# Kernel optimization log

Hardware: AMD Instinct MI355X
Metric: run time of the kernel (lower is better)

## Reference

```python
import jax, jax.numpy as jnp
import numpy as np

V, H, B, T = 8192, 1024, 64, 128

def setup_inputs() -> dict:
    key = jax.random.key(0)
    ks = jax.random.split(key, 7)
    s = 1.0 / np.sqrt(H)                     # torch LSTMCell/Linear default init bound
    xg = np.sqrt(6.0 / (H + V))              # xavier_uniform for fc_out.weight
    return {
        "h0":   jax.random.normal(ks[0], (B, H), jnp.float32),
        "W_ih": jax.random.uniform(ks[1], (4 * H, V), jnp.float32, -s, s),
        "W_hh": jax.random.uniform(ks[2], (4 * H, H), jnp.float32, -s, s),
        "b_ih": jax.random.uniform(ks[3], (4 * H,), jnp.float32, -s, s),
        "b_hh": jax.random.uniform(ks[4], (4 * H,), jnp.float32, -s, s),
        "W_fc": jax.random.uniform(ks[5], (V, H), jnp.float32, -xg, xg),
        "b_fc": jax.random.uniform(ks[6], (V,), jnp.float32, -s, s),
        "max_length": T,
    }

def reference(h0, W_ih, W_hh, b_ih, b_hh, W_fc, b_fc, max_length):
    B_, H_ = h0.shape
    V_ = W_ih.shape[1]
    # hidden state fed to the cell is ALWAYS features[1] (h0) in the original code,
    # so its contribution to the gates is constant across timesteps.
    hh = h0 @ W_hh.T + b_hh + b_ih  # (B, 4H)

    def step(carry, _):
        x, c = carry                          # x: (B,V) accumulated one-hots, c: (B,H)
        gates = x @ W_ih.T + hh               # (B, 4H), torch gate order i,f,g,o
        i, f, g, o = jnp.split(gates, 4, axis=1)
        c = jax.nn.sigmoid(f) * c + jax.nn.sigmoid(i) * jnp.tanh(g)
        h = jax.nn.sigmoid(o) * jnp.tanh(c)
        out = h @ W_fc.T + b_fc               # (B, V)
        idx = jnp.argmax(out, axis=1)
        x = x + jax.nn.one_hot(idx, V_, dtype=x.dtype)  # +1 at argmax (cumulative)
        return (x, c), out

    init = (jnp.zeros((B_, V_), h0.dtype), jnp.zeros((B_, H_), h0.dtype))
    _, outs = jax.lax.scan(step, init, None, length=max_length)  # (T, B, V)
    return jnp.transpose(outs, (1, 2, 0))  # (B, V, T)
```

## Files before the change

kernel.cpp:

```cpp
#include <hip/hip_runtime.h>
#include <math.h>

#define VDIM 8192
#define HDIM 1024
#define BDIM 64
#define TDIM 128
#define H4   4096
#define TCH  16

__device__ __forceinline__ float sigf(float x){ return 1.0f/(1.0f + expf(-x)); }

__device__ __forceinline__ unsigned long long packmax(float v, int vidx){
    unsigned int u = __float_as_uint(v);
    u = (u & 0x80000000u) ? ~u : (u | 0x80000000u);
    return ((unsigned long long)u << 32) | (unsigned int)(VDIM - 1 - vidx);
}

__global__ void __launch_bounds__(256)
hh_kernel(const float* __restrict__ h0, const float* __restrict__ W_hh,
          const float* __restrict__ b_ih, const float* __restrict__ b_hh,
          float* __restrict__ gates)
{
    int blk = blockIdx.x;
    int b = blk >> 4;
    int j = (blk & 15)*256 + threadIdx.x;
    const float* hr = h0 + (size_t)b*HDIM;
    const float* wr = W_hh + (size_t)j*HDIM;
    float s = 0.f;
    for (int k = 0; k < HDIM; k += 4){
        float4 hv = *(const float4*)(hr + k);
        float4 wv = *(const float4*)(wr + k);
        s = fmaf(hv.x, wv.x, s); s = fmaf(hv.y, wv.y, s);
        s = fmaf(hv.z, wv.z, s); s = fmaf(hv.w, wv.w, s);
    }
    gates[(size_t)b*H4 + j] = s + b_ih[j] + b_hh[j];
}

__global__ void __launch_bounds__(256)
cell0_kernel(const float* __restrict__ gates, float* __restrict__ cbuf,
             float* __restrict__ hbuf)
{
    int b = blockIdx.x, u = threadIdx.x*4;
    const float* gb = gates + (size_t)b*H4;
    float4 gi = *(const float4*)(gb + u);
    float4 gf = *(const float4*)(gb + 1024 + u);
    float4 gg = *(const float4*)(gb + 2048 + u);
    float4 go = *(const float4*)(gb + 3072 + u);
    (void)gf;
    float4 c4, h4;
    c4.x = sigf(gi.x)*tanhf(gg.x); c4.y = sigf(gi.y)*tanhf(gg.y);
    c4.z = sigf(gi.z)*tanhf(gg.z); c4.w = sigf(gi.w)*tanhf(gg.w);
    h4.x = sigf(go.x)*tanhf(c4.x); h4.y = sigf(go.y)*tanhf(c4.y);
    h4.z = sigf(go.z)*tanhf(c4.z); h4.w = sigf(go.w)*tanhf(c4.w);
    *(float4*)(cbuf + (size_t)b*HDIM + u) = c4;
    *(float4*)(hbuf + (size_t)b*HDIM + u) = h4;
}

__global__ void __launch_bounds__(256)
tr_kernel(const float* __restrict__ W, float* __restrict__ WT)
{
    __shared__ float tile[64][65];
    const int jb = blockIdx.x * 64;
    const int vb = blockIdx.y * 64;
    const int tx = threadIdx.x & 63;
    const int ty = threadIdx.x >> 6;
    #pragma unroll
    for (int k = 0; k < 64; k += 4)
        tile[ty + k][tx] = W[(size_t)(jb + ty + k)*VDIM + vb + tx];
    __syncthreads();
    #pragma unroll
    for (int k = 0; k < 64; k += 4)
        WT[(size_t)(vb + ty + k)*H4 + jb + tx] = tile[tx][ty + k];
}

__global__ void __launch_bounds__(512, 2)
fc_kernel(const float* __restrict__ W_fc, const float* __restrict__ b_fc,
          const float* __restrict__ hbuf, float* __restrict__ out,
          float* __restrict__ stage,
          unsigned long long* __restrict__ pmax, int t)
{
    __shared__ float buf[8*2048];
    __shared__ unsigned long long bmax[512];
    const int tid = threadIdx.x;
    const int blk = blockIdx.x;
    const int vbase = blk * 32;
    const int g  = tid >> 5;
    const int s  = tid & 31;
    const int b0 = (s >> 2) * 8;
    const int v0 = (s & 3) * 8;
    const int k0 = g * 64;

    float acc[8][8];
    #pragma unroll
    for (int i=0;i<8;++i){
        #pragma unroll
        for (int j=0;j<8;++j) acc[i][j] = 0.f;
    }

    const float* hb = hbuf + (size_t)b0*HDIM + k0;
    const float* wb = W_fc + (size_t)(vbase + v0)*HDIM + k0;

    #pragma unroll 2
    for (int kc = 0; kc < 16; ++kc){
        float4 h4[8], w4[8];
        #pragma unroll
        for (int i=0;i<8;++i) h4[i] = *(const float4*)(hb + (size_t)i*HDIM + kc*4);
        #pragma unroll
        for (int j=0;j<8;++j) w4[j] = *(const float4*)(wb + (size_t)j*HDIM + kc*4);
        #pragma unroll
        for (int i=0;i<8;++i){
            #pragma unroll
            for (int j=0;j<8;++j){
                acc[i][j] = fmaf(h4[i].x, w4[j].x, acc[i][j]);
                acc[i][j] = fmaf(h4[i].y, w4[j].y, acc[i][j]);
                acc[i][j] = fmaf(h4[i].z, w4[j].z, acc[i][j]);
                acc[i][j] = fmaf(h4[i].w, w4[j].w, acc[i][j]);
            }
        }
    }

    for (int half = 8; half >= 1; half >>= 1){
        if (g >= half && g < 2*half){
            float* bp = buf + (g - half)*2048;
            #pragma unroll
            for (int i=0;i<8;++i)
                #pragma unroll
                for (int j=0;j<8;++j) bp[(b0+i)*32 + v0 + j] = acc[i][j];
        }
        __syncthreads();
        if (g < half){
            const float* bp = buf + g*2048;
            #pragma unroll
            for (int i=0;i<8;++i)
                #pragma unroll
                for (int j=0;j<8;++j) acc[i][j] += bp[(b0+i)*32 + v0 + j];
        }
        __syncthreads();
    }
    if (g == 0){
        #pragma unroll
        for (int i=0;i<8;++i)
            #pragma unroll
            for (int j=0;j<8;++j) buf[(b0+i)*32 + v0 + j] = acc[i][j];
    }
    __syncthreads();

    {
        int b  = tid >> 3;
        int vv = (tid & 7) * 4;
        float4 r = *(float4*)(buf + b*32 + vv);
        int v = vbase + vv;
        r.x += b_fc[v]; r.y += b_fc[v+1]; r.z += b_fc[v+2]; r.w += b_fc[v+3];
        if (stage){
            *(float4*)(stage + (((size_t)(t & (TCH-1))*BDIM + b)*VDIM + v)) = r;
        } else {
            float* ob = out + ((size_t)b*VDIM + v)*TDIM + t;
            ob[0] = r.x; ob[TDIM] = r.y; ob[2*TDIM] = r.z; ob[3*TDIM] = r.w;
        }
        unsigned long long m  = packmax(r.x, v);
        unsigned long long m2 = packmax(r.y, v+1); if (m2 > m) m = m2;
        m2 = packmax(r.z, v+2); if (m2 > m) m = m2;
        m2 = packmax(r.w, v+3); if (m2 > m) m = m2;
        bmax[tid] = m;
        __syncthreads();
        if (tid < 64){
            unsigned long long mm = bmax[tid*8];
            #pragma unroll
            for (int q=1;q<8;++q){ unsigned long long z = bmax[tid*8+q]; if (z > mm) mm = z; }
            pmax[(size_t)tid*256 + blk] = mm;
        }
    }
}

__global__ void __launch_bounds__(256)
flush_kernel(const float* __restrict__ stage, float* __restrict__ out, int t0)
{
    const size_t n = (size_t)blockIdx.x*256 + threadIdx.x;
    const int b = (int)(n >> 13);
    const int v = (int)(n & (VDIM-1));
    const size_t st = (size_t)BDIM*VDIM;
    const float* sp = stage + (size_t)b*VDIM + v;
    float* op = out + ((size_t)b*VDIM + v)*TDIM + t0;
    float4 o0, o1, o2, o3;
    o0.x = sp[0*st];  o0.y = sp[1*st];  o0.z = sp[2*st];  o0.w = sp[3*st];
    o1.x = sp[4*st];  o1.y = sp[5*st];  o1.z = sp[6*st];  o1.w = sp[7*st];
    o2.x = sp[8*st];  o2.y = sp[9*st];  o2.z = sp[10*st]; o2.w = sp[11*st];
    o3.x = sp[12*st]; o3.y = sp[13*st]; o3.z = sp[14*st]; o3.w = sp[15*st];
    *(float4*)(op + 0)  = o0;
    *(float4*)(op + 4)  = o1;
    *(float4*)(op + 8)  = o2;
    *(float4*)(op + 12) = o3;
}

__global__ void __launch_bounds__(256)
cell_kernel(const float* __restrict__ W_ih, const float* __restrict__ W_ihT,
            float* __restrict__ gates, float* __restrict__ cbuf,
            float* __restrict__ hbuf, const unsigned long long* __restrict__ pmax)
{
    __shared__ float gbuf[H4];
    __shared__ unsigned long long red[256];
    const int b = blockIdx.x, tid = threadIdx.x;

    red[tid] = pmax[(size_t)b*256 + tid];
    __syncthreads();
    for (int st = 128; st; st >>= 1){
        if (tid < st){ if (red[tid+st] > red[tid]) red[tid] = red[tid+st]; }
        __syncthreads();
    }
    const int idx = VDIM - 1 - (int)(unsigned int)(red[0] & 0xffffffffULL);

    float* gb = gates + (size_t)b*H4;
    if (W_ihT){
        const float* row = W_ihT + (size_t)idx*H4;
        #pragma unroll
        for (int q = 0; q < 4; ++q){
            int j4 = q*1024 + tid*4;
            float4 wv = *(const float4*)(row + j4);
            float4 gv = *(const float4*)(gb + j4);
            gv.x += wv.x; gv.y += wv.y; gv.z += wv.z; gv.w += wv.w;
            *(float4*)(gb + j4) = gv;
            *(float4*)(gbuf + j4) = gv;
        }
    } else {
        #pragma unroll
        for (int q = 0; q < 16; ++q){
            int j = q*256 + tid;
            float gv = gb[j] + W_ih[(size_t)j*VDIM + idx];
            gb[j] = gv;
            gbuf[j] = gv;
        }
    }
    __syncthreads();

    int u = tid*4;
    float4 gi = *(float4*)(gbuf + u);
    float4 gf = *(float4*)(gbuf + 1024 + u);
    float4 gg = *(float4*)(gbuf + 2048 + u);
    float4 go = *(float4*)(gbuf + 3072 + u);
    float4 c4 = *(float4*)(cbuf + (size_t)b*HDIM + u);
    c4.x = sigf(gf.x)*c4.x + sigf(gi.x)*tanhf(gg.x);
    c4.y = sigf(gf.y)*c4.y + sigf(gi.y)*tanhf(gg.y);
    c4.z = sigf(gf.z)*c4.z + sigf(gi.z)*tanhf(gg.z);
    c4.w = sigf(gf.w)*c4.w + sigf(gi.w)*tanhf(gg.w);
    float4 h4;
    h4.x = sigf(go.x)*tanhf(c4.x); h4.y = sigf(go.y)*tanhf(c4.y);
    h4.z = sigf(go.z)*tanhf(c4.z); h4.w = sigf(go.w)*tanhf(c4.w);
    *(float4*)(cbuf + (size_t)b*HDIM + u) = c4;
    *(float4*)(hbuf + (size_t)b*HDIM + u) = h4;
}

extern "C" void kernel_launch(void* const* d_in, const int* in_sizes, int n_in,
                              void* d_out, int out_size, void* d_ws, size_t ws_size,
                              hipStream_t stream)
{
    const float* h0   = (const float*)d_in[0];
    const float* W_ih = (const float*)d_in[1];
    const float* W_hh = (const float*)d_in[2];
    const float* b_ih = (const float*)d_in[3];
    const float* b_hh = (const float*)d_in[4];
    const float* W_fc = (const float*)d_in[5];
    const float* b_fc = (const float*)d_in[6];
    float* out = (float*)d_out;

    float* gates = (float*)d_ws;
    float* cbuf  = gates + (size_t)BDIM*H4;
    float* hbuf  = cbuf  + (size_t)BDIM*HDIM;
    unsigned long long* pmax = (unsigned long long*)(hbuf + (size_t)BDIM*HDIM);

    size_t off = (size_t)BDIM*H4*4 + 2*(size_t)BDIM*HDIM*4 + (size_t)BDIM*256*8;
    const size_t STAGE_B = (size_t)TCH*BDIM*VDIM*4;
    const size_t WT_B    = (size_t)VDIM*H4*4;
    float* stage = nullptr;
    float* wT    = nullptr;
    if (ws_size >= off + STAGE_B){ stage = (float*)((char*)d_ws + off); off += STAGE_B; }
    if (ws_size >= off + WT_B)   { wT    = (float*)((char*)d_ws + off); off += WT_B; }

    hipLaunchKernelGGL(hh_kernel, dim3(1024), dim3(256), 0, stream,
                       h0, W_hh, b_ih, b_hh, gates);
    hipLaunchKernelGGL(cell0_kernel, dim3(64), dim3(256), 0, stream,
                       gates, cbuf, hbuf);
    if (wT){
        hipLaunchKernelGGL(tr_kernel, dim3(64, 128), dim3(256), 0, stream,
                           W_ih, wT);
    }

    for (int t = 0; t < TDIM; ++t){
        hipLaunchKernelGGL(fc_kernel, dim3(256), dim3(512), 0, stream,
                           W_fc, b_fc, hbuf, out, stage, pmax, t);
        if (stage && (t & (TCH-1)) == (TCH-1)){
            hipLaunchKernelGGL(flush_kernel, dim3(BDIM*VDIM/256), dim3(256), 0, stream,
                               stage, out, t - (TCH-1));
        }
        if (t < TDIM - 1){
            hipLaunchKernelGGL(cell_kernel, dim3(64), dim3(256), 0, stream,
                               W_ih, wT, gates, cbuf, hbuf, pmax);
        }
    }
}
```

Measured before the change: 7.292 ms.

## Fuse per-timestep kernels into one persistent cooperative kernel with grid syncs

Replaces the host loop of fc, flush and cell kernel launches per timestep with a single cooperative loop_kernel that runs all 128 timesteps. Grid-wide barriers separate the FC and argmax phase, the cell update and the periodic stage flush. This removes roughly 270 kernel launches and their inter-kernel gaps. In exchange it pays for two grid.sync calls per step, keeps all 256 blocks resident, and shares one block shape across phases that previously used different launch configurations. It falls back to the old path if the cooperative launch fails.

```diff
diff --git a/kernel.cpp b/kernel.cpp
--- a/kernel.cpp
+++ b/kernel.cpp
@@ -1,5 +1,8 @@
 #include <hip/hip_runtime.h>
+#include <hip/hip_cooperative_groups.h>
 #include <math.h>
+
+namespace cg = cooperative_groups;
 
 #define VDIM 8192
 #define HDIM 1024
@@ -73,11 +76,177 @@
         WT[(size_t)(vb + ty + k)*H4 + jb + tx] = tile[tx][ty + k];
 }
 
+__global__ void __launch_bounds__(512)
+loop_kernel(const float* __restrict__ W_fc, const float* __restrict__ b_fc,
+            const float* __restrict__ W_ihT, float* __restrict__ out,
+            float* __restrict__ stage, float* __restrict__ gates,
+            float* __restrict__ cbuf, float* __restrict__ hbuf,
+            unsigned long long* __restrict__ pmax)
+{
+    cg::grid_group grid = cg::this_grid();
+    __shared__ float buf[8*2048];
+    __shared__ unsigned long long bmax[512];
+
+    const int tid = threadIdx.x;
+    const int blk = blockIdx.x;
+    const int vbase = blk * 32;
+    const int g  = tid >> 5;
+    const int s  = tid & 31;
+    const int b0 = (s >> 2) * 8;
+    const int v0 = (s & 3) * 8;
+    const int k0 = g * 64;
+    const int cb = blk & 63;
+    const int cq = blk >> 6;
+
+    const float* hb = hbuf + (size_t)b0*HDIM + k0;
+    const float* wb = W_fc + (size_t)(vbase + v0)*HDIM + k0;
+
+    for (int t = 0; t < TDIM; ++t){
+        float acc[8][8];
+        #pragma unroll
+        for (int i=0;i<8;++i){
+            #pragma unroll
+            for (int j=0;j<8;++j) acc[i][j] = 0.f;
+        }
+
+        #pragma unroll 2
+        for (int kc = 0; kc < 16; ++kc){
+            float4 h4[8], w4[8];
+            #pragma unroll
+            for (int i=0;i<8;++i) h4[i] = *(const float4*)(hb + (size_t)i*HDIM + kc*4);
+            #pragma unroll
+            for (int j=0;j<8;++j) w4[j] = *(const float4*)(wb + (size_t)j*HDIM + kc*4);
+            #pragma unroll
+            for (int i=0;i<8;++i){
+                #pragma unroll
+                for (int j=0;j<8;++j){
+                    acc[i][j] = fmaf(h4[i].x, w4[j].x, acc[i][j]);
+                    acc[i][j] = fmaf(h4[i].y, w4[j].y, acc[i][j]);
+                    acc[i][j] = fmaf(h4[i].z, w4[j].z, acc[i][j]);
+                    acc[i][j] = fmaf(h4[i].w, w4[j].w, acc[i][j]);
+                }
+            }
+        }
+
+        for (int half = 8; half >= 1; half >>= 1){
+            if (g >= half && g < 2*half){
+                float* bp = buf + (g - half)*2048;
+                #pragma unroll
+                for (int i=0;i<8;++i)
+                    #pragma unroll
+                    for (int j=0;j<8;++j) bp[(b0+i)*32 + v0 + j] = acc[i][j];
+            }
+            __syncthreads();
+            if (g < half){
+                const float* bp = buf + g*2048;
+                #pragma unroll
+                for (int i=0;i<8;++i)
+                    #pragma unroll
+                    for (int j=0;j<8;++j) acc[i][j] += bp[(b0+i)*32 + v0 + j];
+            }
+            __syncthreads();
+        }
+        if (g == 0){
+            #pragma unroll
+            for (int i=0;i<8;++i)
+                #pragma unroll
+                for (int j=0;j<8;++j) buf[(b0+i)*32 + v0 + j] = acc[i][j];
+        }
+        __syncthreads();
+
+        {
+            int eb = tid >> 3;
+            int vv = (tid & 7) * 4;
+            float4 r = *(float4*)(buf + eb*32 + vv);
+            int v = vbase + vv;
+            r.x += b_fc[v]; r.y += b_fc[v+1]; r.z += b_fc[v+2]; r.w += b_fc[v+3];
+            *(float4*)(stage + (((size_t)(t & (TCH-1))*BDIM + eb)*VDIM + v)) = r;
+            unsigned long long m  = packmax(r.x, v);
+            unsigned long long m2 = packmax(r.y, v+1); if (m2 > m) m = m2;
+            m2 = packmax(r.z, v+2); if (m2 > m) m = m2;
+            m2 = packmax(r.w, v+3); if (m2 > m) m = m2;
+            bmax[tid] = m;
+            __syncthreads();
+            if (tid < 64){
+                unsigned long long mm = bmax[tid*8];
+                #pragma unroll
+                for (int q=1;q<8;++q){ unsigned long long z = bmax[tid*8+q]; if (z > mm) mm = z; }
+                pmax[(size_t)tid*256 + blk] = mm;
+            }
+        }
+
+        grid.sync();
+
+        if (t < TDIM - 1){
+            if (tid < 256) bmax[tid] = pmax[(size_t)cb*256 + tid];
+            __syncthreads();
+            for (int st = 128; st; st >>= 1){
+                if (tid < st){ if (bmax[tid+st] > bmax[tid]) bmax[tid] = bmax[tid+st]; }
+                __syncthreads();
+            }
+            const int idx = VDIM - 1 - (int)(unsigned int)(bmax[0] & 0xffffffffULL);
+
+            if (tid < 64){
+                const int u = cq*256 + tid*4;
+                const float* row = W_ihT + (size_t)idx*H4;
+                float* gb = gates + (size_t)cb*H4;
+                float4 gi = *(float4*)(gb + u);
+                float4 gf = *(float4*)(gb + 1024 + u);
+                float4 gg = *(float4*)(gb + 2048 + u);
+                float4 go = *(float4*)(gb + 3072 + u);
+                float4 wi = *(const float4*)(row + u);
+                float4 wf = *(const float4*)(row + 1024 + u);
+                float4 wg = *(const float4*)(row + 2048 + u);
+                float4 wo = *(const float4*)(row + 3072 + u);
+                gi.x += wi.x; gi.y += wi.y; gi.z += wi.z; gi.w += wi.w;
+                gf.x += wf.x; gf.y += wf.y; gf.z += wf.z; gf.w += wf.w;
+                gg.x += wg.x; gg.y += wg.y; gg.z += wg.z; gg.w += wg.w;
+                go.x += wo.x; go.y += wo.y; go.z += wo.z; go.w += wo.w;
+                *(float4*)(gb + u)        = gi;
+                *(float4*)(gb + 1024 + u) = gf;
+                *(float4*)(gb + 2048 + u) = gg;
+                *(float4*)(gb + 3072 + u) = go;
+                float4 c4 = *(float4*)(cbuf + (size_t)cb*HDIM + u);
+                c4.x = sigf(gf.x)*c4.x + sigf(gi.x)*tanhf(gg.x);
+                c4.y = sigf(gf.y)*c4.y + sigf(gi.y)*tanhf(gg.y);
+                c4.z = sigf(gf.z)*c4.z + sigf(gi.z)*tanhf(gg.z);
+                c4.w = sigf(gf.w)*c4.w + sigf(gi.w)*tanhf(gg.w);
+                float4 h4;
+                h4.x = sigf(go.x)*tanhf(c4.x); h4.y = sigf(go.y)*tanhf(c4.y);
+                h4.z = sigf(go.z)*tanhf(c4.z); h4.w = sigf(go.w)*tanhf(c4.w);
+                *(float4*)(cbuf + (size_t)cb*HDIM + u) = c4;
+                *(float4*)(hbuf + (size_t)cb*HDIM + u) = h4;
+            }
+        }
+
+        if ((t & (TCH-1)) == (TCH-1)){
+            const int t0 = t - (TCH-1);
+            for (int n = blk*512 + tid; n < BDIM*VDIM; n += 256*512){
+                const int fb = n >> 13;
+                const int fv = n & (VDIM-1);
+                const size_t st = (size_t)BDIM*VDIM;
+                const float* sp = stage + (size_t)fb*VDIM + fv;
+                float* op = out + ((size_t)fb*VDIM + fv)*TDIM + t0;
+                float4 o0, o1, o2, o3;
+                o0.x = sp[0*st];  o0.y = sp[1*st];  o0.z = sp[2*st];  o0.w = sp[3*st];
+                o1.x = sp[4*st];  o1.y = sp[5*st];  o1.z = sp[6*st];  o1.w = sp[7*st];
+                o2.x = sp[8*st];  o2.y = sp[9*st];  o2.z = sp[10*st]; o2.w = sp[11*st];
+                o3.x = sp[12*st]; o3.y = sp[13*st]; o3.z = sp[14*st]; o3.w = sp[15*st];
+                *(float4*)(op + 0)  = o0;
+                *(float4*)(op + 4)  = o1;
+                *(float4*)(op + 8)  = o2;
+                *(float4*)(op + 12) = o3;
+            }
+        }
+
+        grid.sync();
+    }
+}
+
 __global__ void __launch_bounds__(512, 2)
 fc_kernel(const float* __restrict__ W_fc, const float* __restrict__ b_fc,
           const float* __restrict__ hbuf, float* __restrict__ out,
-          float* __restrict__ stage,
-          unsigned long long* __restrict__ pmax, int t)
+          float* __restrict__ stage, unsigned long long* __restrict__ pmax, int t)
 {
     __shared__ float buf[8*2048];
     __shared__ unsigned long long bmax[512];
@@ -96,10 +265,8 @@
         #pragma unroll
         for (int j=0;j<8;++j) acc[i][j] = 0.f;
     }
-
     const float* hb = hbuf + (size_t)b0*HDIM + k0;
     const float* wb = W_fc + (size_t)(vbase + v0)*HDIM + k0;
-
     #pragma unroll 2
     for (int kc = 0; kc < 16; ++kc){
         float4 h4[8], w4[8];
@@ -118,7 +285,6 @@
             }
         }
     }
-
     for (int half = 8; half >= 1; half >>= 1){
         if (g >= half && g < 2*half){
             float* bp = buf + (g - half)*2048;
@@ -144,7 +310,6 @@
             for (int j=0;j<8;++j) buf[(b0+i)*32 + v0 + j] = acc[i][j];
     }
     __syncthreads();
-
     {
         int b  = tid >> 3;
         int vv = (tid & 7) * 4;
@@ -284,16 +449,29 @@
                            W_ih, wT);
     }
 
-    for (int t = 0; t < TDIM; ++t){
-        hipLaunchKernelGGL(fc_kernel, dim3(256), dim3(512), 0, stream,
-                           W_fc, b_fc, hbuf, out, stage, pmax, t);
-        if (stage && (t & (TCH-1)) == (TCH-1)){
-            hipLaunchKernelGGL(flush_kernel, dim3(BDIM*VDIM/256), dim3(256), 0, stream,
-                               stage, out, t - (TCH-1));
-        }
-        if (t < TDIM - 1){
-            hipLaunchKernelGGL(cell_kernel, dim3(64), dim3(256), 0, stream,
-                               W_ih, wT, gates, cbuf, hbuf, pmax);
-        }
-    }
-}
+    bool coop_done = false;
+    if (stage && wT){
+        void* args[] = { (void*)&W_fc, (void*)&b_fc, (void*)&wT, (void*)&out,
+                         (void*)&stage, (void*)&gates, (void*)&cbuf, (void*)&hbuf,
+                         (void*)&pmax };
+        hipError_t e = hipLaunchCooperativeKernel((const void*)loop_kernel,
+                                                  dim3(256), dim3(512),
+                                                  args, 0, stream);
+        if (e == hipSuccess) coop_done = true;
+    }
+
+    if (!coop_done){
+        for (int t = 0; t < TDIM; ++t){
+            hipLaunchKernelGGL(fc_kernel, dim3(256), dim3(512), 0, stream,
+                               W_fc, b_fc, hbuf, out, stage, pmax, t);
+            if (stage && (t & (TCH-1)) == (TCH-1)){
+                hipLaunchKernelGGL(flush_kernel, dim3(BDIM*VDIM/256), dim3(256), 0, stream,
+                                   stage, out, t - (TCH-1));
+            }
+            if (t < TDIM - 1){
+                hipLaunchKernelGGL(cell_kernel, dim3(64), dim3(256), 0, stream,
+                                   W_ih, wT, gates, cbuf, hbuf, pmax);
+            }
+        }
+    }
+}
```

New measurement: 14.33 ms. 1.96x slower.

## Split FC GEMV across 512 blocks and replace tree reduction with one-shot smem reduce

Applied to the files above, without the earlier changes.

The per-step FC kernel now has each block cover 16 vocabulary rows instead of 32, which doubles the grid to 512 blocks and halves per-thread accumulators to raise occupancy. The log-step shared-memory split-K reduction with many barriers is replaced by a single padded shared-memory dump followed by 256 threads each summing all 16 partials. The argmax partial buffer grows to 512 entries per batch row, and the cell kernel folds two entries per thread. In exchange, each h tile is re-read by twice as many blocks and the reduction uses more shared memory per block.

```diff
diff --git a/kernel.cpp b/kernel.cpp
--- a/kernel.cpp
+++ b/kernel.cpp
@@ -7,6 +7,8 @@
 #define TDIM 128
 #define H4   4096
 #define TCH  16
+#define NFC  512
+#define GS   1088
 
 __device__ __forceinline__ float sigf(float x){ return 1.0f/(1.0f + expf(-x)); }
 
@@ -73,28 +75,28 @@
         WT[(size_t)(vb + ty + k)*H4 + jb + tx] = tile[tx][ty + k];
 }
 
-__global__ void __launch_bounds__(512, 2)
+__global__ void __launch_bounds__(512, 4)
 fc_kernel(const float* __restrict__ W_fc, const float* __restrict__ b_fc,
           const float* __restrict__ hbuf, float* __restrict__ out,
           float* __restrict__ stage,
           unsigned long long* __restrict__ pmax, int t)
 {
-    __shared__ float buf[8*2048];
-    __shared__ unsigned long long bmax[512];
+    __shared__ float buf[16*GS];
+    __shared__ unsigned long long bmax[256];
     const int tid = threadIdx.x;
     const int blk = blockIdx.x;
-    const int vbase = blk * 32;
+    const int vbase = blk * 16;
     const int g  = tid >> 5;
     const int s  = tid & 31;
     const int b0 = (s >> 2) * 8;
-    const int v0 = (s & 3) * 8;
+    const int v0 = (s & 3) * 4;
     const int k0 = g * 64;
 
-    float acc[8][8];
+    float acc[8][4];
     #pragma unroll
     for (int i=0;i<8;++i){
         #pragma unroll
-        for (int j=0;j<8;++j) acc[i][j] = 0.f;
+        for (int j=0;j<4;++j) acc[i][j] = 0.f;
     }
 
     const float* hb = hbuf + (size_t)b0*HDIM + k0;
@@ -102,15 +104,15 @@
 
     #pragma unroll 2
     for (int kc = 0; kc < 16; ++kc){
-        float4 h4[8], w4[8];
+        float4 h4[8], w4[4];
         #pragma unroll
         for (int i=0;i<8;++i) h4[i] = *(const float4*)(hb + (size_t)i*HDIM + kc*4);
         #pragma unroll
-        for (int j=0;j<8;++j) w4[j] = *(const float4*)(wb + (size_t)j*HDIM + kc*4);
+        for (int j=0;j<4;++j) w4[j] = *(const float4*)(wb + (size_t)j*HDIM + kc*4);
         #pragma unroll
         for (int i=0;i<8;++i){
             #pragma unroll
-            for (int j=0;j<8;++j){
+            for (int j=0;j<4;++j){
                 acc[i][j] = fmaf(h4[i].x, w4[j].x, acc[i][j]);
                 acc[i][j] = fmaf(h4[i].y, w4[j].y, acc[i][j]);
                 acc[i][j] = fmaf(h4[i].z, w4[j].z, acc[i][j]);
@@ -119,42 +121,42 @@
         }
     }
 
-    for (int half = 8; half >= 1; half >>= 1){
-        if (g >= half && g < 2*half){
-            float* bp = buf + (g - half)*2048;
+    {
+        float* bp = buf + g*GS;
+        #pragma unroll
+        for (int i=0;i<8;++i){
             #pragma unroll
-            for (int i=0;i<8;++i)
-                #pragma unroll
-                for (int j=0;j<8;++j) bp[(b0+i)*32 + v0 + j] = acc[i][j];
-        }
-        __syncthreads();
-        if (g < half){
-            const float* bp = buf + g*2048;
+            for (int j=0;j<4;++j) bp[(b0+i)*17 + v0 + j] = acc[i][j];
+        }
+    }
+    __syncthreads();
+
+    if (tid < 256){
+        const int eb = tid >> 2;
+        const int vv = (tid & 3) * 4;
+        float4 rr[16];
+        #pragma unroll
+        for (int q=0;q<16;++q){
+            const float* bp = buf + q*GS + eb*17 + vv;
+            rr[q].x = bp[0]; rr[q].y = bp[1]; rr[q].z = bp[2]; rr[q].w = bp[3];
+        }
+        #pragma unroll
+        for (int half = 8; half >= 1; half >>= 1){
             #pragma unroll
-            for (int i=0;i<8;++i)
-                #pragma unroll
-                for (int j=0;j<8;++j) acc[i][j] += bp[(b0+i)*32 + v0 + j];
-        }
-        __syncthreads();
-    }
-    if (g == 0){
-        #pragma unroll
-        for (int i=0;i<8;++i)
-            #pragma unroll
-            for (int j=0;j<8;++j) buf[(b0+i)*32 + v0 + j] = acc[i][j];
-    }
-    __syncthreads();
-
-    {
-        int b  = tid >> 3;
-        int vv = (tid & 7) * 4;
-        float4 r = *(float4*)(buf + b*32 + vv);
-        int v = vbase + vv;
+            for (int i=0;i<8;++i){
+                if (i < half){
+                    rr[i].x += rr[i+half].x; rr[i].y += rr[i+half].y;
+                    rr[i].z += rr[i+half].z; rr[i].w += rr[i+half].w;
+                }
+            }
+        }
+        float4 r = rr[0];
+        const int v = vbase + vv;
         r.x += b_fc[v]; r.y += b_fc[v+1]; r.z += b_fc[v+2]; r.w += b_fc[v+3];
         if (stage){
-            *(float4*)(stage + (((size_t)(t & (TCH-1))*BDIM + b)*VDIM + v)) = r;
+            *(float4*)(stage + (((size_t)(t & (TCH-1))*BDIM + eb)*VDIM + v)) = r;
         } else {
-            float* ob = out + ((size_t)b*VDIM + v)*TDIM + t;
+            float* ob = out + ((size_t)eb*VDIM + v)*TDIM + t;
             ob[0] = r.x; ob[TDIM] = r.y; ob[2*TDIM] = r.z; ob[3*TDIM] = r.w;
         }
         unsigned long long m  = packmax(r.x, v);
@@ -162,13 +164,13 @@
         m2 = packmax(r.z, v+2); if (m2 > m) m = m2;
         m2 = packmax(r.w, v+3); if (m2 > m) m = m2;
         bmax[tid] = m;
-        __syncthreads();
-        if (tid < 64){
-            unsigned long long mm = bmax[tid*8];
-            #pragma unroll
-            for (int q=1;q<8;++q){ unsigned long long z = bmax[tid*8+q]; if (z > mm) mm = z; }
-            pmax[(size_t)tid*256 + blk] = mm;
-        }
+    }
+    __syncthreads();
+    if (tid < 64){
+        unsigned long long mm = bmax[tid*4];
+        #pragma unroll
+        for (int q=1;q<4;++q){ unsigned long long z = bmax[tid*4+q]; if (z > mm) mm = z; }
+        pmax[(size_t)tid*NFC + blk] = mm;
     }
 }
 
@@ -201,7 +203,11 @@
     __shared__ unsigned long long red[256];
     const int b = blockIdx.x, tid = threadIdx.x;
 
-    red[tid] = pmax[(size_t)b*256 + tid];
+    {
+        unsigned long long a = pmax[(size_t)b*NFC + tid];
+        unsigned long long c = pmax[(size_t)b*NFC + tid + 256];
+        red[tid] = (c > a) ? c : a;
+    }
     __syncthreads();
     for (int st = 128; st; st >>= 1){
         if (tid < st){ if (red[tid+st] > red[tid]) red[tid] = red[tid+st]; }
@@ -267,7 +273,7 @@
     float* hbuf  = cbuf  + (size_t)BDIM*HDIM;
     unsigned long long* pmax = (unsigned long long*)(hbuf + (size_t)BDIM*HDIM);
 
-    size_t off = (size_t)BDIM*H4*4 + 2*(size_t)BDIM*HDIM*4 + (size_t)BDIM*256*8;
+    size_t off = (size_t)BDIM*H4*4 + 2*(size_t)BDIM*HDIM*4 + (size_t)BDIM*NFC*8;
     const size_t STAGE_B = (size_t)TCH*BDIM*VDIM*4;
     const size_t WT_B    = (size_t)VDIM*H4*4;
     float* stage = nullptr;
@@ -285,7 +291,7 @@
     }
 
     for (int t = 0; t < TDIM; ++t){
-        hipLaunchKernelGGL(fc_kernel, dim3(256), dim3(512), 0, stream,
+        hipLaunchKernelGGL(fc_kernel, dim3(NFC), dim3(512), 0, stream,
                            W_fc, b_fc, hbuf, out, stage, pmax, t);
         if (stage && (t & (TCH-1)) == (TCH-1)){
             hipLaunchKernelGGL(flush_kernel, dim3(BDIM*VDIM/256), dim3(256), 0, stream,
```

Measured after the change: 7.987 ms. 1.1x slower.
